# Kernel tuning notes

Hardware: AMD Instinct MI355X
Metric: run time of the kernel (lower is better)

The kernel has to match this reference:

```python
import jax, jax.numpy as jnp
import numpy as np

# Fixed-shape (jit-compatible) isosurface extraction. The original module calls
# mcubes.marching_cubes on CPU, which has data-dependent output shapes. Here we
# implement the same math (zero-isosurface of -level with linear edge
# interpolation, vertices returned in normalized [0,1]^3 coords with axes
# swapped [2,1,0]) via a marching-tetrahedra decomposition with PADDED outputs:
# a dense vertex buffer (one slot per tet-edge) plus triangle indices and a
# validity mask instead of stream compaction.

RES = 64

# cube corner numbering (offsets in array-index space)
CUBE_OFF = np.array([[0,0,0],[1,0,0],[1,1,0],[0,1,0],
                     [0,0,1],[1,0,1],[1,1,1],[0,1,1]], dtype=np.int32)
# 6-tetrahedra split of the cube around diagonal 0-6
TETS = np.array([[0,5,1,6],[0,1,2,6],[0,2,3,6],
                 [0,3,7,6],[0,7,4,6],[0,4,5,6]], dtype=np.int32)
# tet edges (pairs of tet-local vertex ids)
EDGES = np.array([[0,1],[1,2],[2,0],[0,3],[1,3],[2,3]], dtype=np.int32)

# marching-tetrahedra triangle table: case -> up to 2 triangles of edge ids
_CASES = {1:[[0,3,2]], 2:[[0,1,4]], 3:[[2,3,4],[2,4,1]], 4:[[1,5,2]],
          5:[[0,1,5],[0,5,3]], 6:[[0,4,5],[0,5,2]], 7:[[3,4,5]], 8:[[3,5,4]],
          9:[[0,2,5],[0,5,4]], 10:[[0,3,5],[0,5,1]], 11:[[1,2,5]],
          12:[[1,4,3],[1,3,2]], 13:[[0,4,1]], 14:[[0,2,3]]}
TET_TRIS = np.full((16,2,3), -1, dtype=np.int32)
for c, tris in _CASES.items():
    for i, tr in enumerate(tris):
        TET_TRIS[c, i] = tr


def setup_inputs() -> dict:
    key = jax.random.key(0)
    level = jax.random.normal(key, (RES**3,), dtype=jnp.float32)
    return {"level": level}


def reference(level):
    R = RES
    f = -level.reshape(R, R, R)  # original negates before extraction
    C = (R - 1) ** 3
    # corner scalar values per cell: [C, 8]
    cf = jnp.stack([f[o[0]:o[0]+R-1, o[1]:o[1]+R-1, o[2]:o[2]+R-1].reshape(-1)
                    for o in CUBE_OFF], axis=-1)
    # corner positions per cell in array-index space: [C, 8, 3]
    ax = jnp.arange(R - 1)
    base = jnp.stack(jnp.meshgrid(ax, ax, ax, indexing='ij'), -1).reshape(-1, 1, 3)
    cp = (base + CUBE_OFF[None]).astype(f.dtype)
    # gather per-tet values/positions: [C,6,4], [C,6,4,3]
    fv = cf[:, TETS]
    pv = cp[:, TETS]
    # classification: 4-bit case per tet, bit set where value > 0
    case = ((fv > 0).astype(jnp.int32) * np.array([1, 2, 4, 8], dtype=np.int32)).sum(-1)  # [C,6]
    # linear interpolation on every tet edge (padded; unused slots are garbage)
    fa = fv[..., EDGES[:, 0]]; fb = fv[..., EDGES[:, 1]]          # [C,6,6]
    pa = pv[:, :, EDGES[:, 0]]; pb = pv[:, :, EDGES[:, 1]]        # [C,6,6,3]
    d = fa - fb
    d_safe = jnp.where(jnp.abs(d) < 1e-8, 1e-8, d)
    t = jnp.clip(fa / d_safe, 0.0, 1.0)
    v = pa + t[..., None] * (pb - pa)                              # [C,6,6,3]
    # swap axes (a0,a1,a2)->(a2,a1,a0) and normalize to [0,1], as in original
    v_pos = v.reshape(-1, 3)[:, ::-1] / (R - 1.0)                  # [C*36, 3]
    # triangle emission via table lookup, padded to 2 tris/tet
    te = TET_TRIS[case]                                            # [C,6,2,3]
    valid = te[..., 0] >= 0                                        # [C,6,2]
    base_e = (jnp.arange(C * 6, dtype=jnp.int32) * 6).reshape(C, 6, 1, 1)
    tri = base_e + jnp.maximum(te, 0)                              # [C,6,2,3]
    return v_pos, tri.reshape(-1, 3), valid.reshape(-1)
```

## Files before the change

### kernel.cpp

```cpp
#include <hip/hip_runtime.h>

#define RES       64
#define CM1       63
#define NCELL     250047
#define NTET      1500282
#define V_ELEMS   27005076
#define TRI_ELEMS 9001692

#define TPB 256

__constant__ int c_TETS[6][4] = {
    {0,5,1,6},{0,1,2,6},{0,2,3,6},{0,3,7,6},{0,7,4,6},{0,4,5,6}
};
__constant__ int c_OFF[8][3] = {
    {0,0,0},{1,0,0},{1,1,0},{0,1,0},{0,0,1},{1,0,1},{1,1,1},{0,1,1}
};
__constant__ int c_TRI[16][6] = {
    {-1,-1,-1,-1,-1,-1},
    { 0, 3, 2,-1,-1,-1},
    { 0, 1, 4,-1,-1,-1},
    { 2, 3, 4, 2, 4, 1},
    { 1, 5, 2,-1,-1,-1},
    { 0, 1, 5, 0, 5, 3},
    { 0, 4, 5, 0, 5, 2},
    { 3, 4, 5,-1,-1,-1},
    { 3, 5, 4,-1,-1,-1},
    { 0, 2, 5, 0, 5, 4},
    { 0, 3, 5, 0, 5, 1},
    { 1, 2, 5,-1,-1,-1},
    { 1, 4, 3, 1, 3, 2},
    { 0, 4, 1,-1,-1,-1},
    { 0, 2, 3,-1,-1,-1},
    {-1,-1,-1,-1,-1,-1}
};

__global__ __launch_bounds__(TPB) void mc_kernel(const float* __restrict__ level,
                                                 float* __restrict__ out)
{
    __shared__ float sv[TPB * 18];
    __shared__ float st[TPB * 6];
    __shared__ float sl[TPB * 2];

    int t  = threadIdx.x;
    int g0 = blockIdx.x * TPB;
    int g  = g0 + t;
    int ntet = NTET - g0; if (ntet > TPB) ntet = TPB;

    if (t < ntet) {
        int cell = g / 6;
        int tet  = g - cell * 6;
        int i    = cell / (CM1 * CM1);
        int rem  = cell - i * (CM1 * CM1);
        int j    = rem / CM1;
        int k    = rem - j * CM1;
        int base = i * (RES * RES) + j * RES + k;

        float fv[4], px[4], py[4], pz[4];
        #pragma unroll
        for (int vi = 0; vi < 4; ++vi) {
            int c  = c_TETS[tet][vi];
            int ox = c_OFF[c][0], oy = c_OFF[c][1], oz = c_OFF[c][2];
            fv[vi] = -level[base + ox * (RES * RES) + oy * RES + oz];
            px[vi] = (float)(i + ox);
            py[vi] = (float)(j + oy);
            pz[vi] = (float)(k + oz);
        }

        int cs = (fv[0] > 0.0f ? 1 : 0) | (fv[1] > 0.0f ? 2 : 0)
               | (fv[2] > 0.0f ? 4 : 0) | (fv[3] > 0.0f ? 8 : 0);

        const int EA[6] = {0, 1, 2, 0, 1, 2};
        const int EB[6] = {1, 2, 0, 3, 3, 3};

        const float inv63 = 1.0f / 63.0f;
        #pragma unroll
        for (int e = 0; e < 6; ++e) {
            int a = EA[e], b = EB[e];
            float fa = fv[a], fb = fv[b];
            float d  = fa - fb;
            float ds = (fabsf(d) < 1e-8f) ? 1e-8f : d;
            float tt = fa / ds;
            tt = fminf(fmaxf(tt, 0.0f), 1.0f);
            float vx = px[a] + tt * (px[b] - px[a]);
            float vy = py[a] + tt * (py[b] - py[a]);
            float vz = pz[a] + tt * (pz[b] - pz[a]);
            sv[t * 18 + e * 3 + 0] = vz * inv63;
            sv[t * 18 + e * 3 + 1] = vy * inv63;
            sv[t * 18 + e * 3 + 2] = vx * inv63;
        }

        int base6 = g * 6;
        #pragma unroll
        for (int tr = 0; tr < 2; ++tr) {
            int t0 = c_TRI[cs][tr * 3 + 0];
            int t1 = c_TRI[cs][tr * 3 + 1];
            int t2 = c_TRI[cs][tr * 3 + 2];
            sl[t * 2 + tr] = (t0 >= 0) ? 1.0f : 0.0f;
            int m0 = t0 > 0 ? t0 : 0;
            int m1 = t1 > 0 ? t1 : 0;
            int m2 = t2 > 0 ? t2 : 0;
            st[t * 6 + tr * 3 + 0] = (float)(base6 + m0);
            st[t * 6 + tr * 3 + 1] = (float)(base6 + m1);
            st[t * 6 + tr * 3 + 2] = (float)(base6 + m2);
        }
    }

    __syncthreads();

    {
        int n4 = (ntet * 18) >> 2;
        float4*       gv = (float4*)(out + (size_t)g0 * 18);
        const float4* lv = (const float4*)sv;
        for (int idx = t; idx < n4; idx += TPB) gv[idx] = lv[idx];
    }
    {
        int n4 = (ntet * 6) >> 2;
        float4*       gt = (float4*)(out + V_ELEMS + (size_t)g0 * 6);
        const float4* lt = (const float4*)st;
        for (int idx = t; idx < n4; idx += TPB) gt[idx] = lt[idx];
    }
    {
        int n4 = (ntet * 2) >> 2;
        float4*       gl = (float4*)(out + V_ELEMS + TRI_ELEMS + (size_t)g0 * 2);
        const float4* ll = (const float4*)sl;
        for (int idx = t; idx < n4; idx += TPB) gl[idx] = ll[idx];
    }
}

extern "C" void kernel_launch(void* const* d_in, const int* in_sizes, int n_in,
                              void* d_out, int out_size, void* d_ws, size_t ws_size,
                              hipStream_t stream) {
    const float* level = (const float*)d_in[0];
    float* out = (float*)d_out;
    int blocks = (NTET + TPB - 1) / TPB;
    mc_kernel<<<blocks, TPB, 0, stream>>>(level, out);
}
```

Baseline: 30.85 us.

## Use per-wave shared staging with wave barrier and approximate reciprocal

Each 64-lane wavefront now stages and writes out only its own slice of the shared buffers, so the block-wide __syncthreads becomes a wave barrier. Full waves get an unrolled fixed-count float4 copy loop, and partial waves keep a general loop. The per-edge division is replaced by multiplication with the hardware approximate reciprocal, which can change interpolated positions in the last bits. The wave barrier only orders LDS traffic within a wave, so correctness depends on the compiler waiting for the LDS writes before the reads.

```diff
diff --git a/kernel.cpp b/kernel.cpp
--- a/kernel.cpp
+++ b/kernel.cpp
@@ -42,11 +42,15 @@
     __shared__ float sl[TPB * 2];
 
     int t  = threadIdx.x;
+    int w  = t >> 6;
+    int l  = t & 63;
     int g0 = blockIdx.x * TPB;
     int g  = g0 + t;
     int ntet = NTET - g0; if (ntet > TPB) ntet = TPB;
+    int ntw = ntet - w * 64;
+    ntw = ntw < 0 ? 0 : (ntw > 64 ? 64 : ntw);
 
-    if (t < ntet) {
+    if (l < ntw) {
         int cell = g / 6;
         int tet  = g - cell * 6;
         int i    = cell / (CM1 * CM1);
@@ -79,7 +83,7 @@
             float fa = fv[a], fb = fv[b];
             float d  = fa - fb;
             float ds = (fabsf(d) < 1e-8f) ? 1e-8f : d;
-            float tt = fa / ds;
+            float tt = fa * __builtin_amdgcn_rcpf(ds);
             tt = fminf(fmaxf(tt, 0.0f), 1.0f);
             float vx = px[a] + tt * (px[b] - px[a]);
             float vy = py[a] + tt * (py[b] - py[a]);
@@ -105,25 +109,38 @@
         }
     }
 
-    __syncthreads();
+    __builtin_amdgcn_wave_barrier();
 
-    {
-        int n4 = (ntet * 18) >> 2;
-        float4*       gv = (float4*)(out + (size_t)g0 * 18);
-        const float4* lv = (const float4*)sv;
-        for (int idx = t; idx < n4; idx += TPB) gv[idx] = lv[idx];
-    }
-    {
-        int n4 = (ntet * 6) >> 2;
-        float4*       gt = (float4*)(out + V_ELEMS + (size_t)g0 * 6);
-        const float4* lt = (const float4*)st;
-        for (int idx = t; idx < n4; idx += TPB) gt[idx] = lt[idx];
-    }
-    {
-        int n4 = (ntet * 2) >> 2;
-        float4*       gl = (float4*)(out + V_ELEMS + TRI_ELEMS + (size_t)g0 * 2);
-        const float4* ll = (const float4*)sl;
-        for (int idx = t; idx < n4; idx += TPB) gl[idx] = ll[idx];
+    if (ntw == 64) {
+        float4*       gv = (float4*)(out + (size_t)g0 * 18) + (size_t)w * 288;
+        const float4* lv = (const float4*)sv + w * 288;
+        #pragma unroll
+        for (int n = 0; n < 4; ++n) gv[l + n * 64] = lv[l + n * 64];
+        if (l < 32) gv[l + 256] = lv[l + 256];
+
+        float4*       gt = (float4*)(out + V_ELEMS + (size_t)g0 * 6) + (size_t)w * 96;
+        const float4* lt = (const float4*)st + w * 96;
+        gt[l] = lt[l];
+        if (l < 32) gt[l + 64] = lt[l + 64];
+
+        float4*       gl = (float4*)(out + V_ELEMS + TRI_ELEMS + (size_t)g0 * 2) + (size_t)w * 32;
+        const float4* ll = (const float4*)sl + w * 32;
+        if (l < 32) gl[l] = ll[l];
+    } else if (ntw > 0) {
+        int n4v = (ntw * 18) >> 2;
+        float4*       gv = (float4*)(out + (size_t)g0 * 18) + (size_t)w * 288;
+        const float4* lv = (const float4*)sv + w * 288;
+        for (int idx = l; idx < n4v; idx += 64) gv[idx] = lv[idx];
+
+        int n4t = (ntw * 6) >> 2;
+        float4*       gt = (float4*)(out + V_ELEMS + (size_t)g0 * 6) + (size_t)w * 96;
+        const float4* lt = (const float4*)st + w * 96;
+        for (int idx = l; idx < n4t; idx += 64) gt[idx] = lt[idx];
+
+        int n4l = (ntw * 2) >> 2;
+        float4*       gl = (float4*)(out + V_ELEMS + TRI_ELEMS + (size_t)g0 * 2) + (size_t)w * 32;
+        const float4* ll = (const float4*)sl + w * 32;
+        for (int idx = l; idx < n4l; idx += 64) gl[idx] = ll[idx];
     }
 }
 
```

Result: no change. 30.92 us (+0.2%).
